# Kernel tuning notes

Measured on AMD Instinct MI355X. Metric: run time of the kernel, lower is better.

## Reference

```python
import jax, jax.numpy as jnp
import numpy as np

N_NODES = 100_000
N_EDGES = 3_200_000
F_IN, F_HID, F_OUT = 128, 128, 128
MLP_HID, MLP_OUT = 256, 64


def setup_inputs() -> dict:
    key = jax.random.key(0)
    ks = jax.random.split(key, 11)
    def w(k, shape):
        fan_in = shape[0]
        return jax.random.normal(k, shape, jnp.float32) / jnp.sqrt(jnp.float32(fan_in))
    return {
        'x':   jax.random.normal(ks[0], (N_NODES, F_IN), jnp.float32),
        'src': jax.random.randint(ks[1], (N_EDGES,), 0, N_NODES, jnp.int32),
        'dst': jax.random.randint(ks[2], (N_EDGES,), 0, N_NODES, jnp.int32),
        'w1':  w(ks[3], (F_IN, F_HID)),  'b1': jnp.zeros((F_HID,), jnp.float32),
        'w2':  w(ks[4], (F_HID, F_OUT)), 'b2': jnp.zeros((F_OUT,), jnp.float32),
        'wm1': w(ks[5], (F_OUT, MLP_HID)), 'bm1': jnp.zeros((MLP_HID,), jnp.float32),
        'wm2': w(ks[6], (MLP_HID, MLP_OUT)), 'bm2': jnp.zeros((MLP_OUT,), jnp.float32),
    }


def reference(x, src, dst, w1, b1, w2, b2, wm1, bm1, wm2, bm2):
    n = x.shape[0]
    ones = jnp.ones(src.shape[0], x.dtype)
    # DGL GraphConv norm='both': clamp degrees to >=1, symmetric D^-1/2 A D^-1/2
    out_norm = jnp.clip(jax.ops.segment_sum(ones, src, num_segments=n), 1.0) ** -0.5
    in_norm = jnp.clip(jax.ops.segment_sum(ones, dst, num_segments=n), 1.0) ** -0.5

    def gconv(h, w, b):
        msg = (h * out_norm[:, None])[src]                       # [E, F] gather
        agg = jax.ops.segment_sum(msg, dst, num_segments=n)      # [N, F] scatter-add
        return (agg * in_norm[:, None]) @ w + b

    h = jax.nn.relu(gconv(x, w1, b1))   # conv1 + relu (dropout is identity in eval)
    h = jax.nn.relu(gconv(h, w2, b2))   # conv2 + relu
    h = jax.nn.relu(h @ wm1 + bm1)      # MLP hidden layer
    return h @ wm2 + bm2                # MLP output (no final activation)
```

## Files before the change

### kernel.cpp

```cpp
#include <hip/hip_runtime.h>
#include <hip/hip_bf16.h>
#include <cstdint>

__device__ __forceinline__ unsigned short f2b(float f) {
    union { float f; unsigned int i; } v; v.f = f;
    unsigned int i = v.i;
    unsigned int r = (i + 0x7FFFu + ((i >> 16) & 1u)) >> 16;
    return (unsigned short)r;
}
__device__ __forceinline__ float b2f_lo(unsigned int p) {
    union { unsigned int i; float f; } v; v.i = p << 16; return v.f;
}
__device__ __forceinline__ float b2f_hi(unsigned int p) {
    union { unsigned int i; float f; } v; v.i = p & 0xFFFF0000u; return v.f;
}
__device__ __forceinline__ unsigned int pack2(float a, float b) {
    return (unsigned int)f2b(a) | ((unsigned int)f2b(b) << 16);
}

typedef __attribute__((__ext_vector_type__(8))) __bf16 bf16x8;
typedef __attribute__((__ext_vector_type__(4))) float  f32x4;

#define N_NODES 100000
#define N_EDGES 3200000
#define NBUCK   400
#define BSZ     250
#define NCHUNK  256
#define CHUNK   12500
#define BCAP    9216

__global__ void k_scatter(const int* __restrict__ src, const int* __restrict__ dst,
                          int* __restrict__ gcurA, int* __restrict__ gcurB,
                          unsigned* __restrict__ pairs, unsigned short* __restrict__ keysB,
                          int E) {
    __shared__ int hA[NBUCK], hB[NBUCK], baA[NBUCK], baB[NBUCK], lcA[NBUCK], lcB[NBUCK];
    int t = threadIdx.x, b = blockIdx.x;
    int lo = b * CHUNK, hi = min(lo + CHUNK, E);
    for (int j = t; j < NBUCK; j += 256) { hA[j] = 0; hB[j] = 0; }
    __syncthreads();
    for (int i = lo + t; i < hi; i += 256) {
        atomicAdd(&hA[dst[i] / BSZ], 1);
        atomicAdd(&hB[src[i] / BSZ], 1);
    }
    __syncthreads();
    for (int j = t; j < NBUCK; j += 256) {
        baA[j] = hA[j] ? (j * BCAP + atomicAdd(&gcurA[j], hA[j])) : 0;
        lcA[j] = 0;
        baB[j] = hB[j] ? (j * BCAP + atomicAdd(&gcurB[j], hB[j])) : 0;
        lcB[j] = 0;
    }
    __syncthreads();
    for (int i = lo + t; i < hi; i += 256) {
        int s = src[i], d = dst[i];
        int bA = d / BSZ;
        int l  = atomicAdd(&lcA[bA], 1);
        pairs[baA[bA] + l] = ((unsigned)(d - bA * BSZ) << 17) | (unsigned)s;
        int bB = s / BSZ;
        int l2 = atomicAdd(&lcB[bB], 1);
        keysB[baB[bB] + l2] = (unsigned short)(s - bB * BSZ);
    }
}

__global__ __launch_bounds__(512)
void k_csr_sort(const unsigned* __restrict__ pairs, const int* __restrict__ bcntA,
                int* __restrict__ offsets, int* __restrict__ ends,
                float* __restrict__ in_norm, int* __restrict__ esrc) {
    __shared__ int el[BCAP];
    __shared__ int hist[256], scan[256], curs[256];
    int b = blockIdx.x, t = threadIdx.x;
    int node0 = b * BSZ;
    int bstart = b * BCAP;
    int cnt = bcntA[b];
    int bend = bstart + cnt;
    if (t < 256) hist[t] = 0;
    __syncthreads();
    for (int i = bstart + t; i < bend; i += 512)
        atomicAdd(&hist[pairs[i] >> 17], 1);
    __syncthreads();
    if (t < 256) scan[t] = hist[t];
    __syncthreads();
    for (int d = 1; d < 256; d <<= 1) {
        int v = (t < 256 && t >= d) ? scan[t - d] : 0;
        __syncthreads();
        if (t < 256) scan[t] += v;
        __syncthreads();
    }
    if (t < BSZ) {
        int excl = scan[t] - hist[t];
        offsets[node0 + t] = bstart + excl;
        ends[node0 + t]    = bstart + scan[t];
        in_norm[node0 + t] = rsqrtf((float)max(hist[t], 1));
        curs[t] = excl;
    }
    __syncthreads();
    for (int i = bstart + t; i < bend; i += 512) {
        unsigned p = pairs[i];
        int d = (int)(p >> 17);
        int l = atomicAdd(&curs[d], 1);
        el[l] = (int)(p & 0x1FFFFu);
    }
    __syncthreads();
    int wv = t >> 6, lane = t & 63;
    const int INF = 0x7FFFFFFF;
    for (int n = wv; n < BSZ; n += 8) {
        int len = hist[n];
        if (len <= 1) continue;
        int base = scan[n] - len;
        if (len <= 64) {
            int v0 = (lane < len) ? el[base + lane] : INF;
#pragma unroll
            for (int k = 2; k <= 64; k <<= 1) {
#pragma unroll
                for (int d = 32; d > 0; d >>= 1) {
                    if (d >= k) continue;
                    int w0 = __shfl_xor(v0, d, 64);
                    bool up = ((lane & k) == 0);
                    bool lower = ((lane & d) == 0);
                    v0 = (lower == up) ? min(v0, w0) : max(v0, w0);
                }
            }
            if (lane < len) el[base + lane] = v0;
        } else {
            int v0 = (lane < len) ? el[base + lane] : INF;
            int v1 = (64 + lane < len) ? el[base + 64 + lane] : INF;
#pragma unroll
            for (int k = 2; k <= 128; k <<= 1) {
#pragma unroll
                for (int d = 64; d > 0; d >>= 1) {
                    if (d >= k) continue;
                    if (d == 64) {
                        int a = min(v0, v1), bb = max(v0, v1);
                        v0 = a; v1 = bb;
                    } else {
                        int w0 = __shfl_xor(v0, d, 64);
                        int w1 = __shfl_xor(v1, d, 64);
                        bool up0 = ((lane & k) == 0);
                        bool up1 = (((64 + lane) & k) == 0);
                        bool lower = ((lane & d) == 0);
                        v0 = (lower == up0) ? min(v0, w0) : max(v0, w0);
                        v1 = (lower == up1) ? min(v1, w1) : max(v1, w1);
                    }
                }
            }
            if (lane < len) el[base + lane] = v0;
            if (64 + lane < len) el[base + 64 + lane] = v1;
        }
    }
    __syncthreads();
    for (int i = t; i < cnt; i += 512) esrc[bstart + i] = el[i];
}

__global__ __launch_bounds__(512)
void k_count_scale(const unsigned short* __restrict__ keys,
                   const int* __restrict__ bcntB,
                   const float4* __restrict__ x4, float* __restrict__ out_norm,
                   uint2* __restrict__ xs,
                   const float* __restrict__ w1, const float* __restrict__ w2,
                   const float* __restrict__ wm1, const float* __restrict__ wm2,
                   unsigned short* __restrict__ t1, unsigned short* __restrict__ t2,
                   unsigned short* __restrict__ tm1, unsigned short* __restrict__ tm2) {
    {
        int gid = blockIdx.x * 512 + threadIdx.x;
        if (gid < 81920) {
            const float* w; unsigned short* tt; int Nn, idx;
            if (gid < 16384)       { w = w1;  tt = t1;  Nn = 128; idx = gid; }
            else if (gid < 32768)  { w = w2;  tt = t2;  Nn = 128; idx = gid - 16384; }
            else if (gid < 65536)  { w = wm1; tt = tm1; Nn = 256; idx = gid - 32768; }
            else                   { w = wm2; tt = tm2; Nn = 64;  idx = gid - 65536; }
            int K = (gid < 65536) ? 128 : 256;
            int k = idx / Nn, n = idx - k * Nn;
            tt[(size_t)n * K + k] = f2b(w[idx]);
        }
    }
    __shared__ int hist[256];
    __shared__ float onl[BSZ];
    int b = blockIdx.x, t = threadIdx.x;
    int node0 = b * BSZ;
    int bstart = b * BCAP;
    int bend = bstart + bcntB[b];
    if (t < 256) hist[t] = 0;
    __syncthreads();
    for (int i = bstart + t; i < bend; i += 512)
        atomicAdd(&hist[keys[i]], 1);
    __syncthreads();
    if (t < BSZ) {
        float on = rsqrtf((float)max(hist[t], 1));
        onl[t] = on;
        out_norm[node0 + t] = on;
    }
    __syncthreads();
    size_t base4 = (size_t)node0 * 32;
    for (int i = t; i < BSZ * 32; i += 512) {
        float on = onl[i >> 5];
        float4 v = x4[base4 + i];
        uint2 o;
        o.x = pack2(v.x * on, v.y * on);
        o.y = pack2(v.z * on, v.w * on);
        xs[base4 + i] = o;
    }
}

#define AGG_ADD(p)                                                              \
        a0 += b2f_lo(p.x); a1 += b2f_hi(p.x);                                   \
        a2 += b2f_lo(p.y); a3 += b2f_hi(p.y);                                   \
        a4 += b2f_lo(p.z); a5 += b2f_hi(p.z);                                   \
        a6 += b2f_lo(p.w); a7 += b2f_hi(p.w);

#define AGG_NODE_BODY(node)                                                     \
    int lo = offsets[node], hi = ends[node];                                    \
    float a0 = 0.f, a1 = 0.f, a2 = 0.f, a3 = 0.f,                               \
          a4 = 0.f, a5 = 0.f, a6 = 0.f, a7 = 0.f;                               \
    int k = lo + g;                                                             \
    for (; k + 12 < hi; k += 16) {                                              \
        int s0 = esrc[k];                                                       \
        int s1 = esrc[k + 4];                                                   \
        int s2 = esrc[k + 8];                                                   \
        int s3 = esrc[k + 12];                                                  \
        uint4 p0 = feat[(size_t)s0 * 16 + c];                                   \
        uint4 p1 = feat[(size_t)s1 * 16 + c];                                   \
        uint4 p2 = feat[(size_t)s2 * 16 + c];                                   \
        uint4 p3 = feat[(size_t)s3 * 16 + c];                                   \
        AGG_ADD(p0) AGG_ADD(p1) AGG_ADD(p2) AGG_ADD(p3)                         \
    }                                                                           \
    for (; k < hi; k += 4) {                                                    \
        int s = esrc[k];                                                        \
        uint4 p = feat[(size_t)s * 16 + c];                                     \
        AGG_ADD(p)                                                              \
    }                                                                           \
    a0 += __shfl_xor(a0, 16, 64); a0 += __shfl_xor(a0, 32, 64);                 \
    a1 += __shfl_xor(a1, 16, 64); a1 += __shfl_xor(a1, 32, 64);                 \
    a2 += __shfl_xor(a2, 16, 64); a2 += __shfl_xor(a2, 32, 64);                 \
    a3 += __shfl_xor(a3, 16, 64); a3 += __shfl_xor(a3, 32, 64);                 \
    a4 += __shfl_xor(a4, 16, 64); a4 += __shfl_xor(a4, 32, 64);                 \
    a5 += __shfl_xor(a5, 16, 64); a5 += __shfl_xor(a5, 32, 64);                 \
    a6 += __shfl_xor(a6, 16, 64); a6 += __shfl_xor(a6, 32, 64);                 \
    a7 += __shfl_xor(a7, 16, 64); a7 += __shfl_xor(a7, 32, 64);

__global__ __launch_bounds__(256, 8)
void k_conv(const int* __restrict__ offsets, const int* __restrict__ ends,
            const int* __restrict__ esrc,
            const uint4* __restrict__ feat, const float* __restrict__ in_norm,
            const unsigned short* __restrict__ WT, const float* __restrict__ bias,
            const float* __restrict__ row_scale, unsigned short* __restrict__ C,
            int N) {
    __shared__ __align__(16) unsigned short A[32][136];
    int wv = threadIdx.x >> 6, lane = threadIdx.x & 63;
    int row0 = blockIdx.x * 32;
    int g = lane >> 4, c = lane & 15;

    for (int i = 0; i < 8; ++i) {
        int nl = wv * 8 + i;
        int node = row0 + nl;
        AGG_NODE_BODY(node)
        if (g == 0) {
            float inn = in_norm[node];
            uint4 o;
            o.x = pack2(a0 * inn, a1 * inn);
            o.y = pack2(a2 * inn, a3 * inn);
            o.z = pack2(a4 * inn, a5 * inn);
            o.w = pack2(a6 * inn, a7 * inn);
            *(uint4*)&A[nl][c * 8] = o;
        }
    }
    __syncthreads();

    int m = lane & 15, q = lane >> 4;
    const unsigned short* b0 = WT + (size_t)(wv * 32 + m) * 128 + q * 8;
    const unsigned short* b1 = b0 + (size_t)16 * 128;
    f32x4 acc00 = {0.f, 0.f, 0.f, 0.f}, acc10 = {0.f, 0.f, 0.f, 0.f};
    f32x4 acc01 = {0.f, 0.f, 0.f, 0.f}, acc11 = {0.f, 0.f, 0.f, 0.f};
#pragma unroll
    for (int k = 0; k < 128; k += 32) {
        bf16x8 bf0 = *(const bf16x8*)(b0 + k);
        bf16x8 bf1 = *(const bf16x8*)(b1 + k);
        bf16x8 af0 = *(const bf16x8*)&A[m][q * 8 + k];
        bf16x8 af1 = *(const bf16x8*)&A[16 + m][q * 8 + k];
        acc00 = __builtin_amdgcn_mfma_f32_16x16x32_bf16(af0, bf0, acc00, 0, 0, 0);
        acc10 = __builtin_amdgcn_mfma_f32_16x16x32_bf16(af1, bf0, acc10, 0, 0, 0);
        acc01 = __builtin_amdgcn_mfma_f32_16x16x32_bf16(af0, bf1, acc01, 0, 0, 0);
        acc11 = __builtin_amdgcn_mfma_f32_16x16x32_bf16(af1, bf1, acc11, 0, 0, 0);
    }
    __syncthreads();

    int col0 = wv * 32 + m;
    int col1 = col0 + 16;
    float bc0 = bias[col0], bc1 = bias[col1];
#pragma unroll
    for (int r = 0; r < 4; r++) {
        int rl = q * 4 + r;
        int rr = row0 + rl, rr1 = rr + 16;
        float v00 = fmaxf(acc00[r] + bc0, 0.f);
        float v10 = fmaxf(acc10[r] + bc0, 0.f);
        float v01 = fmaxf(acc01[r] + bc1, 0.f);
        float v11 = fmaxf(acc11[r] + bc1, 0.f);
        float s0 = row_scale[rr], s1 = row_scale[rr1];
        v00 *= s0; v01 *= s0; v10 *= s1; v11 *= s1;
        A[rl][col0]      = f2b(v00);
        A[rl][col1]      = f2b(v01);
        A[rl + 16][col0] = f2b(v10);
        A[rl + 16][col1] = f2b(v11);
    }
    __syncthreads();
#pragma unroll
    for (int it = 0; it < 2; ++it) {
        int idx = it * 256 + (int)threadIdx.x;
        int row = idx >> 4, seg = idx & 15;
        uint4 v = *(const uint4*)&A[row][seg * 8];
        *(uint4*)&C[(size_t)(row0 + row) * 128 + seg * 8] = v;
    }
}

__global__ __launch_bounds__(256, 8)
void k_conv2_mlp(const int* __restrict__ offsets, const int* __restrict__ ends,
                 const int* __restrict__ esrc,
                 const uint4* __restrict__ feat, const float* __restrict__ in_norm,
                 const unsigned short* __restrict__ WT2, const float* __restrict__ b2,
                 const unsigned short* __restrict__ WTM1, const float* __restrict__ bm1,
                 const unsigned short* __restrict__ WTM2, const float* __restrict__ bm2,
                 float* __restrict__ out, int N) {
    __shared__ __align__(16) unsigned short smem[8704];
    unsigned short (*H1)[136] = (unsigned short(*)[136])(smem);
    unsigned short (*A)[136]  = (unsigned short(*)[136])(smem + 4352);
    unsigned short (*H2)[136] = (unsigned short(*)[136])(smem + 4352);

    int wv = threadIdx.x >> 6, lane = threadIdx.x & 63;
    int row0 = blockIdx.x * 32;
    int g = lane >> 4, c = lane & 15;

    for (int i = 0; i < 8; ++i) {
        int nl = wv * 8 + i;
        int node = row0 + nl;
        AGG_NODE_BODY(node)
        if (g == 0) {
            float inn = in_norm[node];
            uint4 o;
            o.x = pack2(a0 * inn, a1 * inn);
            o.y = pack2(a2 * inn, a3 * inn);
            o.z = pack2(a4 * inn, a5 * inn);
            o.w = pack2(a6 * inn, a7 * inn);
            *(uint4*)&A[nl][c * 8] = o;
        }
    }
    __syncthreads();

    int m = lane & 15, q = lane >> 4;

    {
        const unsigned short* bb0 = WT2 + (size_t)(wv * 32 + m) * 128 + q * 8;
        const unsigned short* bb1 = bb0 + (size_t)16 * 128;
        f32x4 acc00 = {0.f, 0.f, 0.f, 0.f}, acc10 = {0.f, 0.f, 0.f, 0.f};
        f32x4 acc01 = {0.f, 0.f, 0.f, 0.f}, acc11 = {0.f, 0.f, 0.f, 0.f};
#pragma unroll
        for (int k = 0; k < 128; k += 32) {
            bf16x8 bf0 = *(const bf16x8*)(bb0 + k);
            bf16x8 bf1 = *(const bf16x8*)(bb1 + k);
            bf16x8 af0 = *(const bf16x8*)&A[m][q * 8 + k];
            bf16x8 af1 = *(const bf16x8*)&A[16 + m][q * 8 + k];
            acc00 = __builtin_amdgcn_mfma_f32_16x16x32_bf16(af0, bf0, acc00, 0, 0, 0);
            acc10 = __builtin_amdgcn_mfma_f32_16x16x32_bf16(af1, bf0, acc10, 0, 0, 0);
            acc01 = __builtin_amdgcn_mfma_f32_16x16x32_bf16(af0, bf1, acc01, 0, 0, 0);
            acc11 = __builtin_amdgcn_mfma_f32_16x16x32_bf16(af1, bf1, acc11, 0, 0, 0);
        }
        int col0 = wv * 32 + m;
        int col1 = col0 + 16;
        float bc0 = b2[col0], bc1 = b2[col1];
#pragma unroll
        for (int r = 0; r < 4; r++) {
            int rl = q * 4 + r;
            H1[rl][col0]      = f2b(fmaxf(acc00[r] + bc0, 0.f));
            H1[rl][col1]      = f2b(fmaxf(acc01[r] + bc1, 0.f));
            H1[rl + 16][col0] = f2b(fmaxf(acc10[r] + bc0, 0.f));
            H1[rl + 16][col1] = f2b(fmaxf(acc11[r] + bc1, 0.f));
        }
    }
    __syncthreads();

    f32x4 macc0 = {0.f, 0.f, 0.f, 0.f}, macc1 = {0.f, 0.f, 0.f, 0.f};
    int colo = wv * 16 + m;
    const unsigned short* bp2 = WTM2 + (size_t)colo * 256 + q * 8;
#pragma unroll
    for (int half = 0; half < 2; ++half) {
#pragma unroll
        for (int cb = 0; cb < 2; cb++) {
            int colh = half * 128 + wv * 32 + cb * 16 + m;
            const unsigned short* bp = WTM1 + (size_t)colh * 128 + q * 8;
            f32x4 acc0 = {0.f, 0.f, 0.f, 0.f};
            f32x4 acc1 = {0.f, 0.f, 0.f, 0.f};
#pragma unroll
            for (int s = 0; s < 4; s++) {
                bf16x8 bfr = *(const bf16x8*)(bp + s * 32);
                bf16x8 ha0 = *(const bf16x8*)&H1[m][s * 32 + q * 8];
                bf16x8 ha1 = *(const bf16x8*)&H1[m + 16][s * 32 + q * 8];
                acc0 = __builtin_amdgcn_mfma_f32_16x16x32_bf16(ha0, bfr, acc0, 0, 0, 0);
                acc1 = __builtin_amdgcn_mfma_f32_16x16x32_bf16(ha1, bfr, acc1, 0, 0, 0);
            }
            float bc = bm1[colh];
            int cl = colh & 127;
#pragma unroll
            for (int r = 0; r < 4; r++) {
                H2[q * 4 + r][cl]      = f2b(fmaxf(acc0[r] + bc, 0.f));
                H2[q * 4 + r + 16][cl] = f2b(fmaxf(acc1[r] + bc, 0.f));
            }
        }
        __syncthreads();
#pragma unroll
        for (int s = 0; s < 4; s++) {
            bf16x8 bfr = *(const bf16x8*)(bp2 + half * 128 + s * 32);
            bf16x8 ha0 = *(const bf16x8*)&H2[m][s * 32 + q * 8];
            bf16x8 ha1 = *(const bf16x8*)&H2[m + 16][s * 32 + q * 8];
            macc0 = __builtin_amdgcn_mfma_f32_16x16x32_bf16(ha0, bfr, macc0, 0, 0, 0);
            macc1 = __builtin_amdgcn_mfma_f32_16x16x32_bf16(ha1, bfr, macc1, 0, 0, 0);
        }
        __syncthreads();
    }

    float* OS = (float*)smem;
    float bc = bm2[colo];
#pragma unroll
    for (int r = 0; r < 4; r++) {
        OS[(q * 4 + r) * 64 + colo]        = macc0[r] + bc;
        OS[(q * 4 + r + 16) * 64 + colo]   = macc1[r] + bc;
    }
    __syncthreads();
#pragma unroll
    for (int it = 0; it < 2; ++it) {
        int idx = it * 256 + (int)threadIdx.x;
        int row = idx >> 4, seg = idx & 15;
        f32x4 v = *(const f32x4*)&OS[row * 64 + seg * 4];
        __builtin_nontemporal_store(v, (f32x4*)&out[(size_t)(row0 + row) * 64 + seg * 4]);
    }
}

extern "C" void kernel_launch(void* const* d_in, const int* in_sizes, int n_in,
                              void* d_out, int out_size, void* d_ws, size_t ws_size,
                              hipStream_t stream) {
    const float* x    = (const float*)d_in[0];
    const int*   src  = (const int*)d_in[1];
    const int*   dst  = (const int*)d_in[2];
    const float* w1   = (const float*)d_in[3];
    const float* b1   = (const float*)d_in[4];
    const float* w2   = (const float*)d_in[5];
    const float* b2   = (const float*)d_in[6];
    const float* wm1  = (const float*)d_in[7];
    const float* bm1  = (const float*)d_in[8];
    const float* wm2  = (const float*)d_in[9];
    const float* bm2  = (const float*)d_in[10];

    const int N = N_NODES;
    const int E = N_EDGES;

    char* p = (char*)d_ws;
    auto alloc = [&](size_t bytes) -> void* {
        void* r = (void*)p;
        p += (bytes + 255) & ~(size_t)255;
        return r;
    };
    int*   gcurA   = (int*)alloc(NBUCK * 4);
    int*   gcurB   = (int*)alloc(NBUCK * 4);
    int*   offsets = (int*)alloc((size_t)N * 4);
    int*   ends    = (int*)alloc((size_t)N * 4);
    float* out_norm = (float*)alloc((size_t)N * 4);
    float* in_norm  = (float*)alloc((size_t)N * 4);
    int*   esrc     = (int*)alloc((size_t)NBUCK * BCAP * 4);
    unsigned int* bufA = (unsigned int*)alloc((size_t)N * 128 * 2);
    unsigned int* bufB = (unsigned int*)alloc((size_t)N * 128 * 2);
    unsigned int* bufC = (unsigned int*)alloc((size_t)N * 128 * 2);
    unsigned short* wt1  = (unsigned short*)alloc(128 * 128 * 2);
    unsigned short* wt2  = (unsigned short*)alloc(128 * 128 * 2);
    unsigned short* wtm1 = (unsigned short*)alloc(256 * 128 * 2);
    unsigned short* wtm2 = (unsigned short*)alloc(64 * 256 * 2);
    (void)ws_size; (void)n_in; (void)in_sizes; (void)out_size;

    unsigned*       pairs = (unsigned*)bufB;
    unsigned short* keysB = (unsigned short*)bufC;

    (void)hipMemsetAsync(gcurA, 0, (size_t)((char*)gcurB - (char*)gcurA) + NBUCK * 4, stream);

    const int TB = 256;
    k_scatter<<<dim3(NCHUNK), dim3(TB), 0, stream>>>(src, dst, gcurA, gcurB,
                                                     pairs, keysB, E);
    k_csr_sort<<<dim3(NBUCK), dim3(512), 0, stream>>>(pairs, gcurA, offsets, ends,
                                                      in_norm, esrc);
    k_count_scale<<<dim3(NBUCK), dim3(512), 0, stream>>>(
        keysB, gcurB, (const float4*)x, out_norm, (uint2*)bufA,
        w1, w2, wm1, wm2, wt1, wt2, wtm1, wtm2);

    k_conv<<<dim3(N / 32), dim3(TB), 0, stream>>>(
        offsets, ends, esrc, (const uint4*)bufA, in_norm, wt1, b1, out_norm,
        (unsigned short*)bufC, N);

    k_conv2_mlp<<<dim3(N / 32), dim3(TB), 0, stream>>>(
        offsets, ends, esrc, (const uint4*)bufC, in_norm, wt2, b2, wtm1, bm1, wtm2, bm2,
        (float*)d_out, N);
}
```

Before: 520.6 us.

## Halve bucket size, widen scatter blocks, merge CSR sort and scaling kernels

Bucket size drops from 250 to 125 nodes, giving 800 buckets, and the per-bucket capacity and shared histogram sizes shrink to match. The scatter kernel now runs 1024-thread blocks. The CSR sort kernel and the out-degree count/scale kernel become one launch of 1600 blocks that branch on block index. This is meant to raise parallelism and occupancy in the build phase and remove one launch, at the cost of more global bucket atomics, and with a smaller capacity margin per bucket that could overflow on skewed graphs.

```diff
diff --git a/kernel.cpp b/kernel.cpp
--- a/kernel.cpp
+++ b/kernel.cpp
@@ -23,34 +23,35 @@
 
 #define N_NODES 100000
 #define N_EDGES 3200000
-#define NBUCK   400
-#define BSZ     250
+#define NBUCK   800
+#define BSZ     125
 #define NCHUNK  256
 #define CHUNK   12500
-#define BCAP    9216
-
-__global__ void k_scatter(const int* __restrict__ src, const int* __restrict__ dst,
-                          int* __restrict__ gcurA, int* __restrict__ gcurB,
-                          unsigned* __restrict__ pairs, unsigned short* __restrict__ keysB,
-                          int E) {
+#define BCAP    4864
+
+__global__ __launch_bounds__(1024)
+void k_scatter(const int* __restrict__ src, const int* __restrict__ dst,
+               int* __restrict__ gcurA, int* __restrict__ gcurB,
+               unsigned* __restrict__ pairs, unsigned short* __restrict__ keysB,
+               int E) {
     __shared__ int hA[NBUCK], hB[NBUCK], baA[NBUCK], baB[NBUCK], lcA[NBUCK], lcB[NBUCK];
     int t = threadIdx.x, b = blockIdx.x;
     int lo = b * CHUNK, hi = min(lo + CHUNK, E);
-    for (int j = t; j < NBUCK; j += 256) { hA[j] = 0; hB[j] = 0; }
-    __syncthreads();
-    for (int i = lo + t; i < hi; i += 256) {
+    for (int j = t; j < NBUCK; j += 1024) { hA[j] = 0; hB[j] = 0; }
+    __syncthreads();
+    for (int i = lo + t; i < hi; i += 1024) {
         atomicAdd(&hA[dst[i] / BSZ], 1);
         atomicAdd(&hB[src[i] / BSZ], 1);
     }
     __syncthreads();
-    for (int j = t; j < NBUCK; j += 256) {
+    for (int j = t; j < NBUCK; j += 1024) {
         baA[j] = hA[j] ? (j * BCAP + atomicAdd(&gcurA[j], hA[j])) : 0;
         lcA[j] = 0;
         baB[j] = hB[j] ? (j * BCAP + atomicAdd(&gcurB[j], hB[j])) : 0;
         lcB[j] = 0;
     }
     __syncthreads();
-    for (int i = lo + t; i < hi; i += 256) {
+    for (int i = lo + t; i < hi; i += 1024) {
         int s = src[i], d = dst[i];
         int bA = d / BSZ;
         int l  = atomicAdd(&lcA[bA], 1);
@@ -62,141 +63,140 @@
 }
 
 __global__ __launch_bounds__(512)
-void k_csr_sort(const unsigned* __restrict__ pairs, const int* __restrict__ bcntA,
-                int* __restrict__ offsets, int* __restrict__ ends,
-                float* __restrict__ in_norm, int* __restrict__ esrc) {
+void k_build2(const unsigned* __restrict__ pairs, const unsigned short* __restrict__ keys,
+              const int* __restrict__ bcntA, const int* __restrict__ bcntB,
+              int* __restrict__ offsets, int* __restrict__ ends,
+              float* __restrict__ in_norm, int* __restrict__ esrc,
+              const float4* __restrict__ x4, float* __restrict__ out_norm,
+              uint2* __restrict__ xs,
+              const float* __restrict__ w1, const float* __restrict__ w2,
+              const float* __restrict__ wm1, const float* __restrict__ wm2,
+              unsigned short* __restrict__ t1, unsigned short* __restrict__ t2,
+              unsigned short* __restrict__ tm1, unsigned short* __restrict__ tm2) {
     __shared__ int el[BCAP];
-    __shared__ int hist[256], scan[256], curs[256];
+    __shared__ int hist[128], scan[128], curs[128];
+    __shared__ float onl[BSZ];
     int b = blockIdx.x, t = threadIdx.x;
-    int node0 = b * BSZ;
-    int bstart = b * BCAP;
-    int cnt = bcntA[b];
-    int bend = bstart + cnt;
-    if (t < 256) hist[t] = 0;
-    __syncthreads();
-    for (int i = bstart + t; i < bend; i += 512)
-        atomicAdd(&hist[pairs[i] >> 17], 1);
-    __syncthreads();
-    if (t < 256) scan[t] = hist[t];
-    __syncthreads();
-    for (int d = 1; d < 256; d <<= 1) {
-        int v = (t < 256 && t >= d) ? scan[t - d] : 0;
-        __syncthreads();
-        if (t < 256) scan[t] += v;
-        __syncthreads();
-    }
-    if (t < BSZ) {
-        int excl = scan[t] - hist[t];
-        offsets[node0 + t] = bstart + excl;
-        ends[node0 + t]    = bstart + scan[t];
-        in_norm[node0 + t] = rsqrtf((float)max(hist[t], 1));
-        curs[t] = excl;
-    }
-    __syncthreads();
-    for (int i = bstart + t; i < bend; i += 512) {
-        unsigned p = pairs[i];
-        int d = (int)(p >> 17);
-        int l = atomicAdd(&curs[d], 1);
-        el[l] = (int)(p & 0x1FFFFu);
-    }
-    __syncthreads();
-    int wv = t >> 6, lane = t & 63;
-    const int INF = 0x7FFFFFFF;
-    for (int n = wv; n < BSZ; n += 8) {
-        int len = hist[n];
-        if (len <= 1) continue;
-        int base = scan[n] - len;
-        if (len <= 64) {
-            int v0 = (lane < len) ? el[base + lane] : INF;
-#pragma unroll
-            for (int k = 2; k <= 64; k <<= 1) {
-#pragma unroll
-                for (int d = 32; d > 0; d >>= 1) {
-                    if (d >= k) continue;
-                    int w0 = __shfl_xor(v0, d, 64);
-                    bool up = ((lane & k) == 0);
-                    bool lower = ((lane & d) == 0);
-                    v0 = (lower == up) ? min(v0, w0) : max(v0, w0);
-                }
-            }
-            if (lane < len) el[base + lane] = v0;
-        } else {
-            int v0 = (lane < len) ? el[base + lane] : INF;
-            int v1 = (64 + lane < len) ? el[base + 64 + lane] : INF;
-#pragma unroll
-            for (int k = 2; k <= 128; k <<= 1) {
-#pragma unroll
-                for (int d = 64; d > 0; d >>= 1) {
-                    if (d >= k) continue;
-                    if (d == 64) {
-                        int a = min(v0, v1), bb = max(v0, v1);
-                        v0 = a; v1 = bb;
-                    } else {
+
+    if (b < NBUCK) {
+        int node0 = b * BSZ;
+        int bstart = b * BCAP;
+        int cnt = bcntA[b];
+        int bend = bstart + cnt;
+        if (t < 128) hist[t] = 0;
+        __syncthreads();
+        for (int i = bstart + t; i < bend; i += 512)
+            atomicAdd(&hist[pairs[i] >> 17], 1);
+        __syncthreads();
+        if (t < 128) scan[t] = hist[t];
+        __syncthreads();
+        for (int d = 1; d < 128; d <<= 1) {
+            int v = (t < 128 && t >= d) ? scan[t - d] : 0;
+            __syncthreads();
+            if (t < 128) scan[t] += v;
+            __syncthreads();
+        }
+        if (t < BSZ) {
+            int excl = scan[t] - hist[t];
+            offsets[node0 + t] = bstart + excl;
+            ends[node0 + t]    = bstart + scan[t];
+            in_norm[node0 + t] = rsqrtf((float)max(hist[t], 1));
+            curs[t] = excl;
+        }
+        __syncthreads();
+        for (int i = bstart + t; i < bend; i += 512) {
+            unsigned p = pairs[i];
+            int d = (int)(p >> 17);
+            int l = atomicAdd(&curs[d], 1);
+            el[l] = (int)(p & 0x1FFFFu);
+        }
+        __syncthreads();
+        int wv = t >> 6, lane = t & 63;
+        const int INF = 0x7FFFFFFF;
+        for (int n = wv; n < BSZ; n += 8) {
+            int len = hist[n];
+            if (len <= 1) continue;
+            int base = scan[n] - len;
+            if (len <= 64) {
+                int v0 = (lane < len) ? el[base + lane] : INF;
+#pragma unroll
+                for (int k = 2; k <= 64; k <<= 1) {
+#pragma unroll
+                    for (int d = 32; d > 0; d >>= 1) {
+                        if (d >= k) continue;
                         int w0 = __shfl_xor(v0, d, 64);
-                        int w1 = __shfl_xor(v1, d, 64);
-                        bool up0 = ((lane & k) == 0);
-                        bool up1 = (((64 + lane) & k) == 0);
+                        bool up = ((lane & k) == 0);
                         bool lower = ((lane & d) == 0);
-                        v0 = (lower == up0) ? min(v0, w0) : max(v0, w0);
-                        v1 = (lower == up1) ? min(v1, w1) : max(v1, w1);
+                        v0 = (lower == up) ? min(v0, w0) : max(v0, w0);
                     }
                 }
+                if (lane < len) el[base + lane] = v0;
+            } else {
+                int v0 = (lane < len) ? el[base + lane] : INF;
+                int v1 = (64 + lane < len) ? el[base + 64 + lane] : INF;
+#pragma unroll
+                for (int k = 2; k <= 128; k <<= 1) {
+#pragma unroll
+                    for (int d = 64; d > 0; d >>= 1) {
+                        if (d >= k) continue;
+                        if (d == 64) {
+                            int a = min(v0, v1), bb = max(v0, v1);
+                            v0 = a; v1 = bb;
+                        } else {
+                            int w0 = __shfl_xor(v0, d, 64);
+                            int w1 = __shfl_xor(v1, d, 64);
+                            bool up0 = ((lane & k) == 0);
+                            bool up1 = (((64 + lane) & k) == 0);
+                            bool lower = ((lane & d) == 0);
+                            v0 = (lower == up0) ? min(v0, w0) : max(v0, w0);
+                            v1 = (lower == up1) ? min(v1, w1) : max(v1, w1);
+                        }
+                    }
+                }
+                if (lane < len) el[base + lane] = v0;
+                if (64 + lane < len) el[base + 64 + lane] = v1;
             }
-            if (lane < len) el[base + lane] = v0;
-            if (64 + lane < len) el[base + 64 + lane] = v1;
-        }
-    }
-    __syncthreads();
-    for (int i = t; i < cnt; i += 512) esrc[bstart + i] = el[i];
-}
-
-__global__ __launch_bounds__(512)
-void k_count_scale(const unsigned short* __restrict__ keys,
-                   const int* __restrict__ bcntB,
-                   const float4* __restrict__ x4, float* __restrict__ out_norm,
-                   uint2* __restrict__ xs,
-                   const float* __restrict__ w1, const float* __restrict__ w2,
-                   const float* __restrict__ wm1, const float* __restrict__ wm2,
-                   unsigned short* __restrict__ t1, unsigned short* __restrict__ t2,
-                   unsigned short* __restrict__ tm1, unsigned short* __restrict__ tm2) {
-    {
-        int gid = blockIdx.x * 512 + threadIdx.x;
-        if (gid < 81920) {
-            const float* w; unsigned short* tt; int Nn, idx;
-            if (gid < 16384)       { w = w1;  tt = t1;  Nn = 128; idx = gid; }
-            else if (gid < 32768)  { w = w2;  tt = t2;  Nn = 128; idx = gid - 16384; }
-            else if (gid < 65536)  { w = wm1; tt = tm1; Nn = 256; idx = gid - 32768; }
-            else                   { w = wm2; tt = tm2; Nn = 64;  idx = gid - 65536; }
-            int K = (gid < 65536) ? 128 : 256;
-            int k = idx / Nn, n = idx - k * Nn;
-            tt[(size_t)n * K + k] = f2b(w[idx]);
-        }
-    }
-    __shared__ int hist[256];
-    __shared__ float onl[BSZ];
-    int b = blockIdx.x, t = threadIdx.x;
-    int node0 = b * BSZ;
-    int bstart = b * BCAP;
-    int bend = bstart + bcntB[b];
-    if (t < 256) hist[t] = 0;
-    __syncthreads();
-    for (int i = bstart + t; i < bend; i += 512)
-        atomicAdd(&hist[keys[i]], 1);
-    __syncthreads();
-    if (t < BSZ) {
-        float on = rsqrtf((float)max(hist[t], 1));
-        onl[t] = on;
-        out_norm[node0 + t] = on;
-    }
-    __syncthreads();
-    size_t base4 = (size_t)node0 * 32;
-    for (int i = t; i < BSZ * 32; i += 512) {
-        float on = onl[i >> 5];
-        float4 v = x4[base4 + i];
-        uint2 o;
-        o.x = pack2(v.x * on, v.y * on);
-        o.y = pack2(v.z * on, v.w * on);
-        xs[base4 + i] = o;
+        }
+        __syncthreads();
+        for (int i = t; i < cnt; i += 512) esrc[bstart + i] = el[i];
+    } else {
+        int bb = b - NBUCK;
+        {
+            int gid = bb * 512 + t;
+            if (gid < 81920) {
+                const float* w; unsigned short* tt; int Nn, idx;
+                if (gid < 16384)       { w = w1;  tt = t1;  Nn = 128; idx = gid; }
+                else if (gid < 32768)  { w = w2;  tt = t2;  Nn = 128; idx = gid - 16384; }
+                else if (gid < 65536)  { w = wm1; tt = tm1; Nn = 256; idx = gid - 32768; }
+                else                   { w = wm2; tt = tm2; Nn = 64;  idx = gid - 65536; }
+                int K = (gid < 65536) ? 128 : 256;
+                int k = idx / Nn, n = idx - k * Nn;
+                tt[(size_t)n * K + k] = f2b(w[idx]);
+            }
+        }
+        int node0 = bb * BSZ;
+        int bstart = bb * BCAP;
+        int bend = bstart + bcntB[bb];
+        if (t < 128) hist[t] = 0;
+        __syncthreads();
+        for (int i = bstart + t; i < bend; i += 512)
+            atomicAdd(&hist[keys[i]], 1);
+        __syncthreads();
+        if (t < BSZ) {
+            float on = rsqrtf((float)max(hist[t], 1));
+            onl[t] = on;
+            out_norm[node0 + t] = on;
+        }
+        __syncthreads();
+        size_t base4 = (size_t)node0 * 32;
+        for (int i = t; i < BSZ * 32; i += 512) {
+            float on = onl[i >> 5];
+            float4 v = x4[base4 + i];
+            uint2 o;
+            o.x = pack2(v.x * on, v.y * on);
+            o.y = pack2(v.z * on, v.w * on);
+            xs[base4 + i] = o;
+        }
     }
 }
 
@@ -477,12 +477,11 @@
     (void)hipMemsetAsync(gcurA, 0, (size_t)((char*)gcurB - (char*)gcurA) + NBUCK * 4, stream);
 
     const int TB = 256;
-    k_scatter<<<dim3(NCHUNK), dim3(TB), 0, stream>>>(src, dst, gcurA, gcurB,
-                                                     pairs, keysB, E);
-    k_csr_sort<<<dim3(NBUCK), dim3(512), 0, stream>>>(pairs, gcurA, offsets, ends,
-                                                      in_norm, esrc);
-    k_count_scale<<<dim3(NBUCK), dim3(512), 0, stream>>>(
-        keysB, gcurB, (const float4*)x, out_norm, (uint2*)bufA,
+    k_scatter<<<dim3(NCHUNK), dim3(1024), 0, stream>>>(src, dst, gcurA, gcurB,
+                                                       pairs, keysB, E);
+    k_build2<<<dim3(2 * NBUCK), dim3(512), 0, stream>>>(
+        pairs, keysB, gcurA, gcurB, offsets, ends, in_norm, esrc,
+        (const float4*)x, out_norm, (uint2*)bufA,
         w1, w2, wm1, wm2, wt1, wt2, wtm1, wtm2);
 
     k_conv<<<dim3(N / 32), dim3(TB), 0, stream>>>(
```

Measured after the change: 487.3 us. 6.4% less time.
